# Performance work log

Measured on AMD Instinct MI355X. Metric: run time of the kernel, lower is better.

Reference implementation:

```python
import jax, jax.numpy as jnp
import numpy as np

NUM_CLASS = 15
STRIDES = (8, 16, 32)
SCALE_FACTOR = 2.0
DELTA = 0.01
DELTA_CONF = 0.01
EPS = 1e-6


def bce_logits(x, t):
    # numerically stable BCEWithLogits, reduction='none'
    return jnp.maximum(x, 0.0) - x * t + jnp.log1p(jnp.exp(-jnp.abs(x)))


def focal(x, t, gamma=2.0, alpha=1.0):
    return alpha * bce_logits(x, t) * jnp.abs(t - jax.nn.sigmoid(x)) ** gamma


def smooth_l1(x, t):
    # torch SmoothL1Loss default beta=1.0, reduction='none'
    n = jnp.abs(x - t)
    return jnp.where(n < 1.0, 0.5 * n * n, n - 0.5)


def giou_xywh(b1, b2):
    # xywh (center) -> xyxy, order-fixed, standard GIOU (utils_basic.GIOU_xywh_torch)
    b1 = jnp.concatenate([b1[..., :2] - b1[..., 2:4] * 0.5, b1[..., :2] + b1[..., 2:4] * 0.5], -1)
    b2 = jnp.concatenate([b2[..., :2] - b2[..., 2:4] * 0.5, b2[..., :2] + b2[..., 2:4] * 0.5], -1)
    b1 = jnp.concatenate([jnp.minimum(b1[..., :2], b1[..., 2:]), jnp.maximum(b1[..., :2], b1[..., 2:])], -1)
    b2 = jnp.concatenate([jnp.minimum(b2[..., :2], b2[..., 2:]), jnp.maximum(b2[..., :2], b2[..., 2:])], -1)
    a1 = (b1[..., 2] - b1[..., 0]) * (b1[..., 3] - b1[..., 1])
    a2 = (b2[..., 2] - b2[..., 0]) * (b2[..., 3] - b2[..., 1])
    lt = jnp.maximum(b1[..., :2], b2[..., :2])
    rb = jnp.minimum(b1[..., 2:], b2[..., 2:])
    wh = jnp.clip(rb - lt, 0.0)
    inter = wh[..., 0] * wh[..., 1]
    union = a1 + a2 - inter
    iou = inter / (union + EPS)
    elt = jnp.minimum(b1[..., :2], b2[..., :2])
    erb = jnp.maximum(b1[..., 2:], b2[..., 2:])
    ewh = jnp.clip(erb - elt, 0.0)
    enclose = ewh[..., 0] * ewh[..., 1]
    return iou - (enclose - union) / (enclose + EPS)


def cal_loss(p1, p1_d, p2, p2_d, label, stride):
    sg = jax.lax.stop_gradient
    batch_size, grid = p1.shape[0], p1.shape[1]
    img_size = float(stride * grid)
    label_xywh = label[..., :4]
    label_l1234 = label[..., 4:8]
    label_a = label[..., 8:12]
    label_r = label[..., 12:13]
    label_mix = label[..., 14:15]
    label_cls = label[..., 16:]

    obj_mask = (label[..., 13:14] == 1).astype(jnp.float32)
    noobj_mask = 1.0 - (label[..., 13:14] != 0).astype(jnp.float32)
    fuzzy_mask = 1.0 - obj_mask - noobj_mask
    gh = jnp.max(label_cls, axis=-1, keepdims=True)

    label_conf_smooth = obj_mask * (1.0 - DELTA_CONF) + DELTA_CONF / 2.0
    cls_nz = (label_cls != 0).astype(jnp.float32)
    label_cls_smooth = cls_nz * (1.0 - DELTA) + DELTA / NUM_CLASS
    area_weight = label[..., 15:16] + (label[..., 15:16] == 0).astype(jnp.float32)
    bbox_loss_scale = SCALE_FACTOR - (SCALE_FACTOR - 1.0) * label_xywh[..., 2:3] * label_xywh[..., 3:4] / (img_size * img_size)

    N = jnp.sum(obj_mask.reshape(batch_size, -1), axis=-1) + 1e-16
    N = jnp.maximum(N, 1.0).reshape(batch_size, 1, 1, 1)

    # ---------------- head 1 ----------------
    p1_d_xywh, p1_d_s, p1_d_r, p1_d_l = p1_d[..., :4], p1_d[..., 4:8], p1_d[..., 8:9], p1_d[..., 9:13]
    p1_conf = p1[..., 9:10]
    xiou1 = giou_xywh(p1_d_xywh, label_xywh)[..., None]
    scores_iou1 = bbox_loss_scale * (1.0 - jnp.clip(xiou1, 0.0, 1.0))
    scores_obb1 = jnp.sum((p1_d_s - label_a) ** 2, axis=-1, keepdims=True)
    scores_area1 = (p1_d_r - label_r) ** 2
    scores_loc1 = jnp.exp(-(scores_iou1 + scores_obb1 + scores_area1))
    offset01 = jnp.max(sg(scores_loc1), axis=-1, keepdims=True)
    g1 = (gh + offset01) / 2.0
    bg_mask1 = noobj_mask + fuzzy_mask * (g1 < 0.3).astype(jnp.float32) * (1.0 - fuzzy_mask * g1)
    fg_mask1 = obj_mask * (g1 >= 0.3).astype(jnp.float32)

    loss_fg1 = fg_mask1 * focal(p1_conf, label_conf_smooth) * label_mix * g1
    loss_bg1 = bg_mask1 * focal(p1_conf, label_conf_smooth) * label_mix
    loss_iou1 = fg_mask1 * scores_iou1 * label_mix * area_weight
    loss_s1 = fg_mask1 * scores_obb1 * label_mix * area_weight
    loss_r1 = fg_mask1 * scores_area1 * label_mix * area_weight
    loss_l1 = fg_mask1 * bbox_loss_scale * smooth_l1(p1_d_l / stride, label_l1234 / stride) * label_mix * area_weight

    loss_fg1 = jnp.sum(loss_fg1 / N) / batch_size * 2
    loss_bg1 = jnp.sum(loss_bg1 / N) / batch_size * 2
    loss_iou1 = jnp.sum(loss_iou1 / N) / batch_size
    loss_s1 = jnp.sum(loss_s1 / N) / batch_size
    loss_r1 = 16 * jnp.sum(loss_r1 / N) / batch_size
    loss_l1 = 0.2 * jnp.sum(loss_l1 / N) / batch_size

    # ---------------- head 2 ----------------
    p2_d_xywh, p2_d_s, p2_d_r, p2_d_l = p2_d[..., :4], p2_d[..., 4:8], p2_d[..., 8:9], p2_d[..., 9:13]
    p2_conf = p2[..., 9:10]
    p2_cls = p2[..., 10:]
    xiou2 = giou_xywh(p2_d_xywh, label_xywh)[..., None]
    scores_iou2 = bbox_loss_scale * (1.0 - jnp.clip(xiou2, 0.0, 1.0))
    scores_obb2 = jnp.sum((p2_d_s - label_a) ** 2, axis=-1, keepdims=True)
    scores_area2 = (p2_d_r - label_r) ** 2
    offset02 = sg(jnp.exp(-(scores_iou2 + scores_obb2 + scores_area2)))
    g2 = (gh + offset02) / 2.0
    bg_mask2 = noobj_mask + fuzzy_mask * (g2 < 0.3).astype(jnp.float32) * (1.0 - fuzzy_mask * g2)
    fg_mask2 = obj_mask * (g2 >= 0.3).astype(jnp.float32)

    loss_fg2 = fg_mask2 * focal(p2_conf, label_conf_smooth) * label_mix * g2
    loss_bg2 = bg_mask2 * focal(p2_conf, label_conf_smooth) * label_mix
    loss_pos2 = cls_nz * obj_mask * bce_logits(p2_cls, label_cls_smooth * offset02) * label_mix * area_weight
    loss_neg2 = (1.0 - cls_nz) * obj_mask * bce_logits(p2_cls, label_cls_smooth) * label_mix * area_weight
    weight_cls2 = jnp.sum(cls_nz * jax.nn.sigmoid(sg(p2_cls)), axis=-1, keepdims=True)
    wg = (weight_cls2 + gh) / 2.0
    loss_iou2 = fg_mask2 * scores_iou2 * label_mix * area_weight * wg
    loss_s2 = fg_mask2 * scores_obb2 * label_mix * area_weight * wg
    loss_r2 = fg_mask2 * scores_area2 * label_mix * area_weight * wg
    loss_l2 = fg_mask2 * bbox_loss_scale * smooth_l1(p2_d_l / stride, label_l1234 / stride) * label_mix * area_weight * wg
    loss_cls2 = fg_mask2 * bce_logits(p2_cls, label_cls_smooth) * label_mix * area_weight

    loss_fg2 = jnp.sum(loss_fg2 / N) / batch_size * 2
    loss_bg2 = jnp.sum(loss_bg2 / N) / batch_size * 2
    loss_pos2 = jnp.sum(loss_pos2 / N) / batch_size * (NUM_CLASS - 1)
    loss_neg2 = jnp.sum(loss_neg2 / N) / batch_size
    loss_iou2 = jnp.sum(loss_iou2 / N) / batch_size
    loss_cls2 = jnp.sum(loss_cls2 / N) / batch_size
    loss_s2 = jnp.sum(loss_s2 / N) / batch_size
    loss_r2 = 16 * jnp.sum(loss_r2 / N) / batch_size
    loss_l2 = 0.2 * jnp.sum(loss_l2 / N) / batch_size

    loss_fg = (loss_fg1 + loss_fg2) / 2
    loss_bg = (loss_bg1 + loss_bg2) / 2
    loss_pos = loss_pos2 * 2
    loss_neg = loss_neg2 * 2
    loss_cls = loss_cls2
    loss_iou = (loss_iou1 + loss_iou2) / 2
    loss_s = (loss_s1 + loss_s2) / 2
    loss_r = (loss_r1 + loss_r2) / 2
    loss_l = (loss_l1 + loss_l2) / 2
    loss = loss_fg + loss_bg + loss_iou + (loss_s + loss_r) + loss_pos + loss_neg + loss_l
    return (loss, loss_fg, loss_bg, loss_pos, loss_neg, loss_iou, loss_cls, loss_s, loss_r, loss_l)


def _make_label(key, B, G, stride):
    ks = jax.random.split(key, 7)
    img = float(G * stride)
    xywh = jax.random.uniform(ks[0], (B, G, G, 4), minval=1.0, maxval=img)
    l1234 = jax.random.uniform(ks[1], (B, G, G, 4), minval=0.0, maxval=img)
    a = jax.random.uniform(ks[2], (B, G, G, 4))
    r = jax.random.uniform(ks[3], (B, G, G, 1))
    flag = jax.random.randint(ks[4], (B, G, G, 1), 0, 3).astype(jnp.float32) / 2.0  # {0,0.5,1}
    mix_area = jax.random.uniform(ks[5], (B, G, G, 2))
    cls_k1, cls_k2 = jax.random.split(ks[6])
    cls = jax.random.uniform(cls_k1, (B, G, G, NUM_CLASS)) * (jax.random.uniform(cls_k2, (B, G, G, NUM_CLASS)) < 0.1)
    return jnp.concatenate([xywh, l1234, a, r, flag, mix_area, cls], -1)


def setup_inputs() -> dict:
    key = jax.random.key(0)
    B = 16
    grids = (128, 64, 32)
    inp = {}
    names = ('s', 'm', 'l')
    for idx, (G, stride, nm) in enumerate(zip(grids, STRIDES, names)):
        ks = jax.random.split(jax.random.fold_in(key, idx), 5)
        inp['p1_' + nm] = jax.random.normal(ks[0], (B, G, G, 10), jnp.float32)
        inp['p1d_' + nm] = jax.random.uniform(ks[1], (B, G, G, 13), minval=0.0, maxval=float(G * stride))
        inp['p2_' + nm] = jax.random.normal(ks[2], (B, G, G, 25), jnp.float32)
        inp['p2d_' + nm] = jax.random.uniform(ks[3], (B, G, G, 13), minval=0.0, maxval=float(G * stride))
        inp['label_' + nm] = _make_label(ks[4], B, G, stride)
    inp['epoch'] = 10
    inp['i'] = 100
    return inp


def reference(p1_s, p1_m, p1_l, p1d_s, p1d_m, p1d_l, p2_s, p2_m, p2_l, p2d_s, p2d_m, p2d_l, label_s, label_m, label_l, epoch, i):
    outs = [
        cal_loss(p1_s, p1d_s, p2_s, p2d_s, label_s, STRIDES[0]),
        cal_loss(p1_m, p1d_m, p2_m, p2d_m, label_m, STRIDES[1]),
        cal_loss(p1_l, p1d_l, p2_l, p2d_l, label_l, STRIDES[2]),
    ]
    totals = [outs[0][k] + outs[1][k] + outs[2][k] for k in range(10)]
    return jnp.stack(totals)  # [loss, fg, bg, pos, neg, iou, cls, s, r, l]
```

## Files before the change

kernel.cpp:

```cpp
#include <hip/hip_runtime.h>
#include <math.h>

#define NC 15

typedef float f4_t __attribute__((ext_vector_type(4)));
typedef f4_t __attribute__((aligned(4))) u4_t;

struct Params {
    const float* p1[3];
    const float* p1d[3];
    const float* p2[3];
    const float* p2d[3];
    const float* lb[3];
    double* sums;
};

__device__ __forceinline__ float rcp_f(float x) { return __builtin_amdgcn_rcpf(x); }

__device__ __forceinline__ float focal_f(float x, float t) {
    float e = __expf(-fabsf(x));
    float rc = rcp_f(1.0f + e);
    float sp = __logf(1.0f + e);
    float bce = fmaxf(x, 0.0f) - x * t + sp;
    float sig = (x >= 0.0f ? 1.0f : e) * rc;
    float d = t - sig;
    return bce * d * d;
}
__device__ __forceinline__ float sl1_f(float x, float t) {
    float n = fabsf(x - t);
    return n < 1.0f ? 0.5f * n * n : n - 0.5f;
}

__device__ __forceinline__ float giou_f(f4_t b, float lx, float ly, float lw, float lh) {
    float b1x0 = b.x - b.z * 0.5f, b1y0 = b.y - b.w * 0.5f;
    float b1x1 = b.x + b.z * 0.5f, b1y1 = b.y + b.w * 0.5f;
    float b2x0 = lx - lw * 0.5f, b2y0 = ly - lh * 0.5f;
    float b2x1 = lx + lw * 0.5f, b2y1 = ly + lh * 0.5f;
    float ax0 = fminf(b1x0, b1x1), ay0 = fminf(b1y0, b1y1);
    float ax1 = fmaxf(b1x0, b1x1), ay1 = fmaxf(b1y0, b1y1);
    float cx0 = fminf(b2x0, b2x1), cy0 = fminf(b2y0, b2y1);
    float cx1 = fmaxf(b2x0, b2x1), cy1 = fmaxf(b2y0, b2y1);
    float a1 = (ax1 - ax0) * (ay1 - ay0);
    float a2 = (cx1 - cx0) * (cy1 - cy0);
    float ltx = fmaxf(ax0, cx0), lty = fmaxf(ay0, cy0);
    float rbx = fminf(ax1, cx1), rby = fminf(ay1, cy1);
    float iw = fmaxf(rbx - ltx, 0.0f), ih = fmaxf(rby - lty, 0.0f);
    float inter = iw * ih;
    float uni = a1 + a2 - inter;
    float iou = inter * rcp_f(uni + 1e-6f);
    float ex0 = fminf(ax0, cx0), ey0 = fminf(ay0, cy0);
    float ex1 = fmaxf(ax1, cx1), ey1 = fmaxf(ay1, cy1);
    float ew = fmaxf(ex1 - ex0, 0.0f), eh = fmaxf(ey1 - ey0, 0.0f);
    float enc = ew * eh;
    return iou - (enc - uni) * rcp_f(enc + 1e-6f);
}

__global__ __launch_bounds__(128, 4) void loss_all(Params P) {
    __shared__ __align__(16) float sL[3968];
    __shared__ float red[2][10];

    int tid = threadIdx.x;
    int bid = blockIdx.x;
    int lvl, lblk, shift;
    float invStride;
    if (bid >= 2560)      { lvl = 2; lblk = bid - 2560; shift = 10; invStride = 1.0f / 32.0f; }
    else if (bid >= 2048) { lvl = 1; lblk = bid - 2048; shift = 12; invStride = 1.0f / 16.0f; }
    else                  { lvl = 0; lblk = bid;        shift = 14; invStride = 1.0f / 8.0f;  }
    int cell0 = lblk << 7;
    int c = cell0 + tid;
    int batch = c >> shift;

    {
        const float4* gLv = (const float4*)(P.lb[lvl] + (size_t)cell0 * 31);
        float4* vL = (float4*)sL;
#pragma unroll
        for (int k = 0; k < 7; ++k) vL[tid + 128 * k] = gLv[tid + 128 * k];
        if (tid < 96) vL[896 + tid] = gLv[896 + tid];
    }

    const float* pa = P.p1d[lvl] + (size_t)c * 13;
    u4_t A0 = *(const u4_t*)(pa + 0);
    u4_t A1 = *(const u4_t*)(pa + 4);
    u4_t A2 = *(const u4_t*)(pa + 8);
    float A3 = pa[12];
    const float* pb = P.p2d[lvl] + (size_t)c * 13;
    u4_t B0 = *(const u4_t*)(pb + 0);
    u4_t B1 = *(const u4_t*)(pb + 4);
    u4_t B2 = *(const u4_t*)(pb + 8);
    float B3 = pb[12];
    const float* pq = P.p2[lvl] + (size_t)c * 25 + 9;
    u4_t Q0 = *(const u4_t*)(pq + 0);
    u4_t Q1 = *(const u4_t*)(pq + 4);
    u4_t Q2 = *(const u4_t*)(pq + 8);
    u4_t Q3 = *(const u4_t*)(pq + 12);
    float conf1 = P.p1[lvl][(size_t)c * 10 + 9];

    __syncthreads();

    const float* L = sL + tid * 31;
    float lx = L[0], ly = L[1], lw = L[2], lh = L[3];
    float l1 = L[4], l2 = L[5], l3 = L[6], l4 = L[7];
    float a0 = L[8], a1 = L[9], a2 = L[10], a3 = L[11];
    float lr = L[12];
    float flag = L[13];
    float mix = L[14];
    float area = L[15];
    float gh = 0.0f;
    unsigned nzm = 0u;
#pragma unroll
    for (int k = 0; k < NC; ++k) {
        float cv = L[16 + k];
        gh = fmaxf(gh, cv);
        if (cv != 0.0f) nzm |= (1u << k);
    }

    float obj   = (flag == 1.0f) ? 1.0f : 0.0f;
    float noobj = (flag == 0.0f) ? 1.0f : 0.0f;
    float fuzzy = 1.0f - obj - noobj;
    float conf_t = obj * 0.99f + 0.005f;
    float aw = area + ((area == 0.0f) ? 1.0f : 0.0f);
    float bls = 2.0f - lw * lh * (1.0f / (1024.0f * 1024.0f));

    float v0, v1, v2, v3, v4, v5, v6, v7, v8, v9;

    {
        float xiou = giou_f(A0, lx, ly, lw, lh);
        float siou = bls * (1.0f - fminf(fmaxf(xiou, 0.0f), 1.0f));
        float d0 = A1.x - a0, d1 = A1.y - a1, d2 = A1.z - a2, d3 = A1.w - a3;
        float sobb = d0 * d0 + d1 * d1 + d2 * d2 + d3 * d3;
        float dr = A2.x - lr;
        float sarea = dr * dr;
        float off = __expf(-(siou + sobb + sarea));
        float g = (gh + off) * 0.5f;
        float bg = noobj + fuzzy * ((g < 0.3f) ? 1.0f : 0.0f) * (1.0f - fuzzy * g);
        float fg = obj * ((g >= 0.3f) ? 1.0f : 0.0f);
        float foc = focal_f(conf1, conf_t);
        float fma_ = fg * mix * aw;
        v0 = fg * foc * mix * g;
        v1 = bg * foc * mix;
        v2 = fma_ * siou;
        v3 = fma_ * sobb;
        v4 = fma_ * sarea;
        float sl = sl1_f(A2.y * invStride, l1 * invStride)
                 + sl1_f(A2.z * invStride, l2 * invStride)
                 + sl1_f(A2.w * invStride, l3 * invStride)
                 + sl1_f(A3 * invStride,   l4 * invStride);
        v5 = fg * bls * sl * mix * aw;
    }

    {
        float xiou = giou_f(B0, lx, ly, lw, lh);
        float siou2 = bls * (1.0f - fminf(fmaxf(xiou, 0.0f), 1.0f));
        float d0 = B1.x - a0, d1 = B1.y - a1, d2 = B1.z - a2, d3 = B1.w - a3;
        float sobb2 = d0 * d0 + d1 * d1 + d2 * d2 + d3 * d3;
        float dr = B2.x - lr;
        float sarea2 = dr * dr;
        float off2 = __expf(-(siou2 + sobb2 + sarea2));
        float sl2 = sl1_f(B2.y * invStride, l1 * invStride)
                  + sl1_f(B2.z * invStride, l2 * invStride)
                  + sl1_f(B2.w * invStride, l3 * invStride)
                  + sl1_f(B3 * invStride,   l4 * invStride);

        float conf2 = Q0.x;
        float g = (gh + off2) * 0.5f;
        float bg = noobj + fuzzy * ((g < 0.3f) ? 1.0f : 0.0f) * (1.0f - fuzzy * g);
        float fg = obj * ((g >= 0.3f) ? 1.0f : 0.0f);
        float foc = focal_f(conf2, conf_t);
        v0 += fg * foc * mix * g;
        v1 += bg * foc * mix;

        float cx[NC] = {Q0.y, Q0.z, Q0.w, Q1.x, Q1.y, Q1.z, Q1.w,
                        Q2.x, Q2.y, Q2.z, Q2.w, Q3.x, Q3.y, Q3.z, Q3.w};
        float pos = 0.0f, neg = 0.0f, wsum = 0.0f, clsb = 0.0f;
#pragma unroll
        for (int k = 0; k < NC; ++k) {
            float x = cx[k];
            bool nz = (nzm >> k) & 1u;
            float smn = (nz ? 0.99f : 0.0f) + (0.01f / 15.0f);
            float e = __expf(-fabsf(x));
            float sp = __logf(1.0f + e);
            float mx = fmaxf(x, 0.0f);
            float b0 = mx - x * smn + sp;
            clsb += b0;
            if (nz) {
                pos += mx - x * (smn * off2) + sp;
                wsum += (x >= 0.0f ? 1.0f : e) * rcp_f(1.0f + e);
            } else {
                neg += b0;
            }
        }
        float wgq = (wsum + gh) * 0.5f;
        float oma = obj * mix * aw;
        v6 = oma * pos;
        v7 = oma * neg;
        float fmaw = fg * mix * aw * wgq;
        v2 += fmaw * siou2;
        v3 += fmaw * sobb2;
        v4 += fmaw * sarea2;
        v5 += fg * bls * sl2 * mix * aw * wgq;
        v8 = fg * clsb * mix * aw;
    }
    v9 = obj;

#pragma unroll
    for (int o = 32; o > 0; o >>= 1) {
        v0 += __shfl_down(v0, o);
        v1 += __shfl_down(v1, o);
        v2 += __shfl_down(v2, o);
        v3 += __shfl_down(v3, o);
        v4 += __shfl_down(v4, o);
        v5 += __shfl_down(v5, o);
        v6 += __shfl_down(v6, o);
        v7 += __shfl_down(v7, o);
        v8 += __shfl_down(v8, o);
        v9 += __shfl_down(v9, o);
    }
    int lane = tid & 63, wid = tid >> 6;
    if (lane == 0) {
        red[wid][0] = v0; red[wid][1] = v1; red[wid][2] = v2; red[wid][3] = v3;
        red[wid][4] = v4; red[wid][5] = v5; red[wid][6] = v6; red[wid][7] = v7;
        red[wid][8] = v8; red[wid][9] = v9;
    }
    __syncthreads();
    if (tid < 10) {
        float total = red[0][tid] + red[1][tid];
        atomicAdd(&P.sums[((size_t)((lvl << 4) + batch)) * 10 + tid], (double)total);
    }
}

__global__ __launch_bounds__(64) void finalize_kernel(const double* __restrict__ S,
                                                      float* __restrict__ out) {
    int lane = threadIdx.x;
    double loc[10];
#pragma unroll
    for (int t = 0; t < 10; ++t) loc[t] = 0.0;
    if (lane < 48) {
        const double* s = S + (size_t)lane * 10;
        double invN = 1.0 / fmax(s[9], 1.0);
#pragma unroll
        for (int t = 0; t < 9; ++t) loc[t] = s[t] * invN;
    }
#pragma unroll
    for (int t = 0; t < 9; ++t) {
#pragma unroll
        for (int o = 32; o > 0; o >>= 1) loc[t] += __shfl_down(loc[t], o);
    }
    if (lane == 0) {
        const double invB = 1.0 / 16.0;
        double fg  = loc[0] * invB;
        double bg  = loc[1] * invB;
        double iou = loc[2] * invB * 0.5;
        double s_  = loc[3] * invB * 0.5;
        double r   = loc[4] * invB * 8.0;
        double l   = loc[5] * invB * 0.1;
        double pos = loc[6] * invB * 28.0;
        double neg = loc[7] * invB * 2.0;
        double cls = loc[8] * invB;
        double loss = fg + bg + iou + s_ + r + pos + neg + l;
        out[0] = (float)loss; out[1] = (float)fg; out[2] = (float)bg;
        out[3] = (float)pos;  out[4] = (float)neg; out[5] = (float)iou;
        out[6] = (float)cls;  out[7] = (float)s_;  out[8] = (float)r;
        out[9] = (float)l;
    }
}

extern "C" void kernel_launch(void* const* d_in, const int* in_sizes, int n_in,
                              void* d_out, int out_size, void* d_ws, size_t ws_size,
                              hipStream_t stream) {
    (void)in_sizes; (void)n_in; (void)out_size; (void)ws_size;
    double* sums = (double*)d_ws;
    hipMemsetAsync(d_ws, 0, 48 * 10 * sizeof(double), stream);

    Params P;
    for (int lvl = 0; lvl < 3; ++lvl) {
        P.p1[lvl]  = (const float*)d_in[lvl * 5 + 0];
        P.p1d[lvl] = (const float*)d_in[lvl * 5 + 1];
        P.p2[lvl]  = (const float*)d_in[lvl * 5 + 2];
        P.p2d[lvl] = (const float*)d_in[lvl * 5 + 3];
        P.lb[lvl]  = (const float*)d_in[lvl * 5 + 4];
    }
    P.sums = sums;

    loss_all<<<dim3(2688), dim3(128), 0, stream>>>(P);
    finalize_kernel<<<dim3(1), dim3(64), 0, stream>>>(sums, (float*)d_out);
}
```

Baseline: 36.12 us.

## Stage all inputs via direct global-to-LDS loads with single-wave blocks

Every input stream (labels, both decode tensors, class logits, conf) is now staged into shared memory with the global_load_lds builtin, giving coalesced 16-byte transfers instead of per-thread strided loads. Blocks shrink to one 64-lane wave, which removes __syncthreads and the cross-wave reduction. Atomics are spread over 8 slots per (level,batch) to cut contention, and the finalize kernel sums those slots. The cost is twice as many blocks, ten atomics per block from lane 0, and unaligned strided LDS reads when each lane picks up its fields.

```diff
diff --git a/kernel.cpp b/kernel.cpp
--- a/kernel.cpp
+++ b/kernel.cpp
@@ -2,9 +2,6 @@
 #include <math.h>
 
 #define NC 15
-
-typedef float f4_t __attribute__((ext_vector_type(4)));
-typedef f4_t __attribute__((aligned(4))) u4_t;
 
 struct Params {
     const float* p1[3];
@@ -17,6 +14,17 @@
 
 __device__ __forceinline__ float rcp_f(float x) { return __builtin_amdgcn_rcpf(x); }
 
+__device__ __forceinline__ void stage16(const float* g, float* l) {
+    __builtin_amdgcn_global_load_lds(
+        (const __attribute__((address_space(1))) void*)g,
+        (__attribute__((address_space(3))) void*)l, 16, 0, 0);
+}
+__device__ __forceinline__ void stage4(const float* g, float* l) {
+    __builtin_amdgcn_global_load_lds(
+        (const __attribute__((address_space(1))) void*)g,
+        (__attribute__((address_space(3))) void*)l, 4, 0, 0);
+}
+
 __device__ __forceinline__ float focal_f(float x, float t) {
     float e = __expf(-fabsf(x));
     float rc = rcp_f(1.0f + e);
@@ -31,9 +39,10 @@
     return n < 1.0f ? 0.5f * n * n : n - 0.5f;
 }
 
-__device__ __forceinline__ float giou_f(f4_t b, float lx, float ly, float lw, float lh) {
-    float b1x0 = b.x - b.z * 0.5f, b1y0 = b.y - b.w * 0.5f;
-    float b1x1 = b.x + b.z * 0.5f, b1y1 = b.y + b.w * 0.5f;
+__device__ __forceinline__ float giou_f(float bx, float by, float bz, float bw,
+                                        float lx, float ly, float lw, float lh) {
+    float b1x0 = bx - bz * 0.5f, b1y0 = by - bw * 0.5f;
+    float b1x1 = bx + bz * 0.5f, b1y1 = by + bw * 0.5f;
     float b2x0 = lx - lw * 0.5f, b2y0 = ly - lh * 0.5f;
     float b2x1 = lx + lw * 0.5f, b2y1 = ly + lh * 0.5f;
     float ax0 = fminf(b1x0, b1x1), ay0 = fminf(b1y0, b1y1);
@@ -55,49 +64,47 @@
     return iou - (enc - uni) * rcp_f(enc + 1e-6f);
 }
 
-__global__ __launch_bounds__(128, 4) void loss_all(Params P) {
-    __shared__ __align__(16) float sL[3968];
-    __shared__ float red[2][10];
-
-    int tid = threadIdx.x;
+__global__ __launch_bounds__(64, 2) void loss_all(Params P) {
+    __shared__ __align__(16) float sL[1984];
+    __shared__ __align__(16) float sA[832];
+    __shared__ __align__(16) float sB[832];
+    __shared__ __align__(16) float sQ[1600];
+    __shared__ __align__(16) float sC[64];
+
+    int lane = threadIdx.x;
     int bid = blockIdx.x;
     int lvl, lblk, shift;
     float invStride;
-    if (bid >= 2560)      { lvl = 2; lblk = bid - 2560; shift = 10; invStride = 1.0f / 32.0f; }
-    else if (bid >= 2048) { lvl = 1; lblk = bid - 2048; shift = 12; invStride = 1.0f / 16.0f; }
+    if (bid >= 5120)      { lvl = 2; lblk = bid - 5120; shift = 10; invStride = 1.0f / 32.0f; }
+    else if (bid >= 4096) { lvl = 1; lblk = bid - 4096; shift = 12; invStride = 1.0f / 16.0f; }
     else                  { lvl = 0; lblk = bid;        shift = 14; invStride = 1.0f / 8.0f;  }
-    int cell0 = lblk << 7;
-    int c = cell0 + tid;
+    int cell0 = lblk << 6;
+    int c = cell0 + lane;
     int batch = c >> shift;
 
-    {
-        const float4* gLv = (const float4*)(P.lb[lvl] + (size_t)cell0 * 31);
-        float4* vL = (float4*)sL;
-#pragma unroll
-        for (int k = 0; k < 7; ++k) vL[tid + 128 * k] = gLv[tid + 128 * k];
-        if (tid < 96) vL[896 + tid] = gLv[896 + tid];
-    }
-
-    const float* pa = P.p1d[lvl] + (size_t)c * 13;
-    u4_t A0 = *(const u4_t*)(pa + 0);
-    u4_t A1 = *(const u4_t*)(pa + 4);
-    u4_t A2 = *(const u4_t*)(pa + 8);
-    float A3 = pa[12];
-    const float* pb = P.p2d[lvl] + (size_t)c * 13;
-    u4_t B0 = *(const u4_t*)(pb + 0);
-    u4_t B1 = *(const u4_t*)(pb + 4);
-    u4_t B2 = *(const u4_t*)(pb + 8);
-    float B3 = pb[12];
-    const float* pq = P.p2[lvl] + (size_t)c * 25 + 9;
-    u4_t Q0 = *(const u4_t*)(pq + 0);
-    u4_t Q1 = *(const u4_t*)(pq + 4);
-    u4_t Q2 = *(const u4_t*)(pq + 8);
-    u4_t Q3 = *(const u4_t*)(pq + 12);
-    float conf1 = P.p1[lvl][(size_t)c * 10 + 9];
-
-    __syncthreads();
-
-    const float* L = sL + tid * 31;
+    const float* gL = P.lb[lvl]  + (size_t)cell0 * 31;
+    const float* gA = P.p1d[lvl] + (size_t)cell0 * 13;
+    const float* gB = P.p2d[lvl] + (size_t)cell0 * 13;
+    const float* gQ = P.p2[lvl]  + (size_t)cell0 * 25;
+
+#pragma unroll
+    for (int k = 0; k < 7; ++k) stage16(gL + (size_t)(k * 64 + lane) * 4, sL + k * 256);
+    if (lane < 48) stage16(gL + (size_t)(448 + lane) * 4, sL + 1792);
+#pragma unroll
+    for (int k = 0; k < 3; ++k) stage16(gA + (size_t)(k * 64 + lane) * 4, sA + k * 256);
+    if (lane < 16) stage16(gA + (size_t)(192 + lane) * 4, sA + 768);
+#pragma unroll
+    for (int k = 0; k < 3; ++k) stage16(gB + (size_t)(k * 64 + lane) * 4, sB + k * 256);
+    if (lane < 16) stage16(gB + (size_t)(192 + lane) * 4, sB + 768);
+#pragma unroll
+    for (int k = 0; k < 6; ++k) stage16(gQ + (size_t)(k * 64 + lane) * 4, sQ + k * 256);
+    if (lane < 16) stage16(gQ + (size_t)(384 + lane) * 4, sQ + 1536);
+    stage4(P.p1[lvl] + (size_t)c * 10 + 9, sC);
+
+    asm volatile("s_waitcnt vmcnt(0)" ::: "memory");
+    __builtin_amdgcn_sched_barrier(0);
+
+    const float* L = sL + lane * 31;
     float lx = L[0], ly = L[1], lw = L[2], lh = L[3];
     float l1 = L[4], l2 = L[5], l3 = L[6], l4 = L[7];
     float a0 = L[8], a1 = L[9], a2 = L[10], a3 = L[11];
@@ -124,44 +131,47 @@
     float v0, v1, v2, v3, v4, v5, v6, v7, v8, v9;
 
     {
-        float xiou = giou_f(A0, lx, ly, lw, lh);
+        const float* A = sA + lane * 13;
+        float xiou = giou_f(A[0], A[1], A[2], A[3], lx, ly, lw, lh);
         float siou = bls * (1.0f - fminf(fmaxf(xiou, 0.0f), 1.0f));
-        float d0 = A1.x - a0, d1 = A1.y - a1, d2 = A1.z - a2, d3 = A1.w - a3;
+        float d0 = A[4] - a0, d1 = A[5] - a1, d2 = A[6] - a2, d3 = A[7] - a3;
         float sobb = d0 * d0 + d1 * d1 + d2 * d2 + d3 * d3;
-        float dr = A2.x - lr;
+        float dr = A[8] - lr;
         float sarea = dr * dr;
         float off = __expf(-(siou + sobb + sarea));
         float g = (gh + off) * 0.5f;
         float bg = noobj + fuzzy * ((g < 0.3f) ? 1.0f : 0.0f) * (1.0f - fuzzy * g);
         float fg = obj * ((g >= 0.3f) ? 1.0f : 0.0f);
-        float foc = focal_f(conf1, conf_t);
+        float foc = focal_f(sC[lane], conf_t);
         float fma_ = fg * mix * aw;
         v0 = fg * foc * mix * g;
         v1 = bg * foc * mix;
         v2 = fma_ * siou;
         v3 = fma_ * sobb;
         v4 = fma_ * sarea;
-        float sl = sl1_f(A2.y * invStride, l1 * invStride)
-                 + sl1_f(A2.z * invStride, l2 * invStride)
-                 + sl1_f(A2.w * invStride, l3 * invStride)
-                 + sl1_f(A3 * invStride,   l4 * invStride);
+        float sl = sl1_f(A[9] * invStride,  l1 * invStride)
+                 + sl1_f(A[10] * invStride, l2 * invStride)
+                 + sl1_f(A[11] * invStride, l3 * invStride)
+                 + sl1_f(A[12] * invStride, l4 * invStride);
         v5 = fg * bls * sl * mix * aw;
     }
 
     {
-        float xiou = giou_f(B0, lx, ly, lw, lh);
+        const float* B = sB + lane * 13;
+        float xiou = giou_f(B[0], B[1], B[2], B[3], lx, ly, lw, lh);
         float siou2 = bls * (1.0f - fminf(fmaxf(xiou, 0.0f), 1.0f));
-        float d0 = B1.x - a0, d1 = B1.y - a1, d2 = B1.z - a2, d3 = B1.w - a3;
+        float d0 = B[4] - a0, d1 = B[5] - a1, d2 = B[6] - a2, d3 = B[7] - a3;
         float sobb2 = d0 * d0 + d1 * d1 + d2 * d2 + d3 * d3;
-        float dr = B2.x - lr;
+        float dr = B[8] - lr;
         float sarea2 = dr * dr;
         float off2 = __expf(-(siou2 + sobb2 + sarea2));
-        float sl2 = sl1_f(B2.y * invStride, l1 * invStride)
-                  + sl1_f(B2.z * invStride, l2 * invStride)
-                  + sl1_f(B2.w * invStride, l3 * invStride)
-                  + sl1_f(B3 * invStride,   l4 * invStride);
-
-        float conf2 = Q0.x;
+        float sl2 = sl1_f(B[9] * invStride,  l1 * invStride)
+                  + sl1_f(B[10] * invStride, l2 * invStride)
+                  + sl1_f(B[11] * invStride, l3 * invStride)
+                  + sl1_f(B[12] * invStride, l4 * invStride);
+
+        const float* Q = sQ + lane * 25 + 9;
+        float conf2 = Q[0];
         float g = (gh + off2) * 0.5f;
         float bg = noobj + fuzzy * ((g < 0.3f) ? 1.0f : 0.0f) * (1.0f - fuzzy * g);
         float fg = obj * ((g >= 0.3f) ? 1.0f : 0.0f);
@@ -169,12 +179,10 @@
         v0 += fg * foc * mix * g;
         v1 += bg * foc * mix;
 
-        float cx[NC] = {Q0.y, Q0.z, Q0.w, Q1.x, Q1.y, Q1.z, Q1.w,
-                        Q2.x, Q2.y, Q2.z, Q2.w, Q3.x, Q3.y, Q3.z, Q3.w};
         float pos = 0.0f, neg = 0.0f, wsum = 0.0f, clsb = 0.0f;
 #pragma unroll
         for (int k = 0; k < NC; ++k) {
-            float x = cx[k];
+            float x = Q[1 + k];
             bool nz = (nzm >> k) & 1u;
             float smn = (nz ? 0.99f : 0.0f) + (0.01f / 15.0f);
             float e = __expf(-fabsf(x));
@@ -215,16 +223,18 @@
         v8 += __shfl_down(v8, o);
         v9 += __shfl_down(v9, o);
     }
-    int lane = tid & 63, wid = tid >> 6;
     if (lane == 0) {
-        red[wid][0] = v0; red[wid][1] = v1; red[wid][2] = v2; red[wid][3] = v3;
-        red[wid][4] = v4; red[wid][5] = v5; red[wid][6] = v6; red[wid][7] = v7;
-        red[wid][8] = v8; red[wid][9] = v9;
-    }
-    __syncthreads();
-    if (tid < 10) {
-        float total = red[0][tid] + red[1][tid];
-        atomicAdd(&P.sums[((size_t)((lvl << 4) + batch)) * 10 + tid], (double)total);
+        double* s = P.sums + ((size_t)(((lvl << 4) + batch) * 8 + (lblk & 7))) * 10;
+        atomicAdd(s + 0, (double)v0);
+        atomicAdd(s + 1, (double)v1);
+        atomicAdd(s + 2, (double)v2);
+        atomicAdd(s + 3, (double)v3);
+        atomicAdd(s + 4, (double)v4);
+        atomicAdd(s + 5, (double)v5);
+        atomicAdd(s + 6, (double)v6);
+        atomicAdd(s + 7, (double)v7);
+        atomicAdd(s + 8, (double)v8);
+        atomicAdd(s + 9, (double)v9);
     }
 }
 
@@ -235,10 +245,16 @@
 #pragma unroll
     for (int t = 0; t < 10; ++t) loc[t] = 0.0;
     if (lane < 48) {
-        const double* s = S + (size_t)lane * 10;
-        double invN = 1.0 / fmax(s[9], 1.0);
-#pragma unroll
-        for (int t = 0; t < 9; ++t) loc[t] = s[t] * invN;
+        const double* s = S + (size_t)lane * 80;
+        double acc[10];
+#pragma unroll
+        for (int t = 0; t < 10; ++t) acc[t] = 0.0;
+        for (int b = 0; b < 8; ++b)
+#pragma unroll
+            for (int t = 0; t < 10; ++t) acc[t] += s[b * 10 + t];
+        double invN = 1.0 / fmax(acc[9], 1.0);
+#pragma unroll
+        for (int t = 0; t < 9; ++t) loc[t] = acc[t] * invN;
     }
 #pragma unroll
     for (int t = 0; t < 9; ++t) {
@@ -269,7 +285,7 @@
                               hipStream_t stream) {
     (void)in_sizes; (void)n_in; (void)out_size; (void)ws_size;
     double* sums = (double*)d_ws;
-    hipMemsetAsync(d_ws, 0, 48 * 10 * sizeof(double), stream);
+    hipMemsetAsync(d_ws, 0, 48 * 8 * 10 * sizeof(double), stream);
 
     Params P;
     for (int lvl = 0; lvl < 3; ++lvl) {
@@ -281,6 +297,6 @@
     }
     P.sums = sums;
 
-    loss_all<<<dim3(2688), dim3(128), 0, stream>>>(P);
+    loss_all<<<dim3(5376), dim3(64), 0, stream>>>(P);
     finalize_kernel<<<dim3(1), dim3(64), 0, stream>>>(sums, (float*)d_out);
 }
```

Result: slower. 48.42 us (+34.1%).
